# Kernel tuning notes

Measured on AMD Instinct MI355X. Metric: run time of the kernel, lower is better.

## Reference

```python
import jax, jax.numpy as jnp
import numpy as np

SLOPE = 25.0  # snntorch surrogate.fast_sigmoid default slope
NUM_STEPS = 15

@jax.custom_vjp
def spike(x):
    # Heaviside forward, fast-sigmoid surrogate backward
    return (x > 0).astype(x.dtype)

def _spike_fwd(x):
    return spike(x), x

def _spike_bwd(x, g):
    return (g / (SLOPE * jnp.abs(x) + 1.0) ** 2,)

spike.defvjp(_spike_fwd, _spike_bwd)


def setup_inputs() -> dict:
    p, hidden, B = 97, 512, 32768
    key = jax.random.key(0)
    ks = jax.random.split(key, 6)
    s1 = 1.0 / np.sqrt(2 * hidden)
    s2 = 1.0 / np.sqrt(hidden)
    return {
        "x": jax.random.randint(ks[0], (B, 2), 0, p, dtype=jnp.int64 if jax.config.jax_enable_x64 else jnp.int32),
        "embed_w": jax.random.normal(ks[1], (p, hidden), jnp.float32),
        "W1": jax.random.uniform(ks[2], (hidden, 2 * hidden), jnp.float32, -s1, s1),
        "b1": jax.random.uniform(ks[3], (hidden,), jnp.float32, -s1, s1),
        "W2": jax.random.uniform(ks[4], (p, hidden), jnp.float32, -s2, s2),
        "b2": jax.random.uniform(ks[5], (p,), jnp.float32, -s2, s2),
        "beta1": jnp.float32(0.85),
        "beta2": jnp.float32(0.85),
        "thr1": jnp.float32(1.0),
        "thr2": jnp.float32(1.0),
    }


def reference(x, embed_w, W1, b1, W2, b2, beta1, beta2, thr1, thr2):
    # parameter clamps (done in-place under no_grad in torch)
    beta1 = jnp.clip(beta1, 0.1, 0.9)
    beta2 = jnp.clip(beta2, 0.1, 0.9)
    thr1 = jnp.maximum(thr1, 0.1)
    thr2 = jnp.maximum(thr2, 0.1)

    B = x.shape[0]
    hidden = embed_w.shape[1]
    p = W2.shape[0]

    emb = embed_w[x].reshape(B, 2 * hidden)          # [B, 2H]
    cur1 = emb @ W1.T + b1                           # constant across steps [B, H]

    def step(carry, _):
        mem1, mem2 = carry
        # lif1: Leaky, reset_mechanism='subtract'; reset computed from prev mem (detached)
        reset = jax.lax.stop_gradient((mem1 - thr1 > 0).astype(mem1.dtype))
        mem1 = jnp.clip(beta1, 0.0, 1.0) * mem1 + cur1 - reset * thr1
        spk1 = spike(mem1 - thr1)                    # [B, H]
        cur2 = spk1 @ W2.T + b2                      # [B, p]
        # lif2: reset_mechanism='none'
        mem2 = jnp.clip(beta2, 0.0, 1.0) * mem2 + cur2
        return (mem1, mem2), None

    mem1 = jnp.zeros((B, hidden), cur1.dtype)
    mem2 = jnp.zeros((B, p), cur1.dtype)
    (mem1, mem2), _ = jax.lax.scan(step, (mem1, mem2), None, length=NUM_STEPS)
    return mem2  # final membrane potential of output layer
```

## Files before the change

kernel.cpp:

```cpp
#include <hip/hip_runtime.h>
#include <cstddef>

#define PMOD 97
#define HID 512
#define NPAIR 9409
#define NSTEPS 15

typedef __attribute__((ext_vector_type(8))) short short8;
typedef __attribute__((ext_vector_type(4))) short short4_t;
typedef __attribute__((ext_vector_type(4))) float f32x4;

static __device__ __forceinline__ unsigned short f2bf_rn(float f) {
    unsigned u = __float_as_uint(f);
    u += 0x7FFFu + ((u >> 16) & 1u);
    return (unsigned short)(u >> 16);
}
static __device__ __forceinline__ float bf2f(unsigned short h) {
    return __uint_as_float(((unsigned)h) << 16);
}

__global__ __launch_bounds__(256) void k_cvt(const float* __restrict__ W1,
                                             const float* __restrict__ embed,
                                             const float* __restrict__ W2,
                                             short* __restrict__ w1hi,
                                             short* __restrict__ w1lo,
                                             short* __restrict__ ehi,
                                             short* __restrict__ elo,
                                             short* __restrict__ w2bf) {
    const int idx = blockIdx.x * 256 + threadIdx.x;
    if (idx < 131072) {
        const float4 v = ((const float4*)W1)[idx];
        const float vv[4] = {v.x, v.y, v.z, v.w};
        short4_t h4, l4;
#pragma unroll
        for (int q = 0; q < 4; ++q) {
            const unsigned short hb = f2bf_rn(vv[q]);
            h4[q] = (short)hb;
            l4[q] = (short)f2bf_rn(vv[q] - bf2f(hb));
        }
        *(short4_t*)(w1hi + idx * 4) = h4;
        *(short4_t*)(w1lo + idx * 4) = l4;
    } else if (idx < 143488) {
        const int k = idx - 131072;
        const float4 v = ((const float4*)embed)[k];
        const float vv[4] = {v.x, v.y, v.z, v.w};
        short4_t h4, l4;
#pragma unroll
        for (int q = 0; q < 4; ++q) {
            const unsigned short hb = f2bf_rn(vv[q]);
            h4[q] = (short)hb;
            l4[q] = (short)f2bf_rn(vv[q] - bf2f(hb));
        }
        *(short4_t*)(ehi + k * 4) = h4;
        *(short4_t*)(elo + k * 4) = l4;
    } else if (idx < 155904) {
        const int k = idx - 143488;
        const float4 v = ((const float4*)W2)[k];
        const float vv[4] = {v.x, v.y, v.z, v.w};
        short4_t h4;
#pragma unroll
        for (int q = 0; q < 4; ++q) h4[q] = (short)f2bf_rn(vv[q]);
        *(short4_t*)(w2bf + k * 4) = h4;
    }
}

__global__ __launch_bounds__(256) void k_abm(const short* __restrict__ ehi,
                                             const short* __restrict__ elo,
                                             const short* __restrict__ w1hi,
                                             const short* __restrict__ w1lo,
                                             const float* __restrict__ b1,
                                             float* __restrict__ Ap,
                                             float* __restrict__ Bm) {
    __shared__ f32x4 red[3][4][64];

    const int t = threadIdx.x;
    const int lane = t & 63;
    const int kq = t >> 6;
    const int mt = blockIdx.x >> 4;
    const int ng = blockIdx.x & 15;

    int e = mt * 16 + (lane & 15);
    if (e > PMOD - 1) e = PMOD - 1;
    const int kbase = kq * 128 + (lane >> 4) * 8;

    f32x4 acc[4];
#pragma unroll
    for (int nt = 0; nt < 4; ++nt) acc[nt] = (f32x4){0.f, 0.f, 0.f, 0.f};

#pragma unroll
    for (int kt = 0; kt < 4; ++kt) {
        const int k = kbase + kt * 32;
        const short8 ahi = *(const short8*)(ehi + (size_t)e * HID + k);
        const short8 alo = *(const short8*)(elo + (size_t)e * HID + k);
#pragma unroll
        for (int nt = 0; nt < 4; ++nt) {
            const int n = ng * 64 + nt * 16 + (lane & 15);
            const int h = n & 511;
            const int half = n >> 9;
            const size_t boff = (size_t)h * 1024 + half * HID + k;
            const short8 bhi = *(const short8*)(w1hi + boff);
            const short8 blo = *(const short8*)(w1lo + boff);
            acc[nt] = __builtin_amdgcn_mfma_f32_16x16x32_bf16(ahi, bhi, acc[nt], 0, 0, 0);
            acc[nt] = __builtin_amdgcn_mfma_f32_16x16x32_bf16(alo, bhi, acc[nt], 0, 0, 0);
            acc[nt] = __builtin_amdgcn_mfma_f32_16x16x32_bf16(ahi, blo, acc[nt], 0, 0, 0);
        }
    }

    if (kq != 0) {
#pragma unroll
        for (int nt = 0; nt < 4; ++nt) red[kq - 1][nt][lane] = acc[nt];
    }
    __syncthreads();
    if (kq == 0) {
#pragma unroll
        for (int nt = 0; nt < 4; ++nt) {
            f32x4 a = acc[nt];
            a += red[0][nt][lane];
            a += red[1][nt][lane];
            a += red[2][nt][lane];
            const int n = ng * 64 + nt * 16 + (lane & 15);
            const int h = n & 511;
            const int half = n >> 9;
            const float bias = half ? 0.f : b1[h];
#pragma unroll
            for (int reg = 0; reg < 4; ++reg) {
                const int er = mt * 16 + (lane >> 4) * 4 + reg;
                if (er < PMOD) {
                    if (half == 0) Ap[(size_t)er * HID + h] = a[reg] + bias;
                    else           Bm[(size_t)er * HID + h] = a[reg];
                }
            }
        }
    }
}

__global__ __launch_bounds__(256) void k_pairs(const float* __restrict__ Ap,
                                               const float* __restrict__ Bm,
                                               const short* __restrict__ w2bf,
                                               const float* __restrict__ b2,
                                               const float* __restrict__ pbeta1,
                                               const float* __restrict__ pbeta2,
                                               const float* __restrict__ pthr1,
                                               float* __restrict__ pairOut) {
    __shared__ f32x4 red[3][7][64];

    const float beta1 = fminf(fmaxf(pbeta1[0], 0.1f), 0.9f);
    const float beta2 = fminf(fmaxf(pbeta2[0], 0.1f), 0.9f);
    const float thr   = fmaxf(pthr1[0], 0.1f);

    const int t = threadIdx.x;
    const int lane = t & 63;
    const int kq = t >> 6;
    const int pblk = blockIdx.x * 16;

    const int pid0 = pblk + (lane & 15);
    const int pid  = (pid0 < NPAIR) ? pid0 : (NPAIR - 1);
    const unsigned i = (unsigned)pid / PMOD;
    const unsigned j = (unsigned)pid - i * PMOD;
    const int kbase = kq * 128 + (lane >> 4) * 8;

    f32x4 acc[7];
#pragma unroll
    for (int nt = 0; nt < 7; ++nt) acc[nt] = (f32x4){0.f, 0.f, 0.f, 0.f};

#pragma unroll
    for (int kt = 0; kt < 4; ++kt) {
        const int k = kbase + kt * 32;
        const float* ap = Ap + (size_t)i * HID + k;
        const float* bp = Bm + (size_t)j * HID + k;
        const float4 a0 = *(const float4*)ap;
        const float4 a1 = *(const float4*)(ap + 4);
        const float4 g0 = *(const float4*)bp;
        const float4 g1 = *(const float4*)(bp + 4);
        float c[8] = {a0.x + g0.x, a0.y + g0.y, a0.z + g0.z, a0.w + g0.w,
                      a1.x + g1.x, a1.y + g1.y, a1.z + g1.z, a1.w + g1.w};
        float cm[8], m[8], w[8];
        bool sb[8];
#pragma unroll
        for (int q = 0; q < 8; ++q) {
            cm[q] = c[q] - thr; m[q] = 0.f; w[q] = 0.f; sb[q] = false;
        }
        for (int s = 0; s < NSTEPS; ++s) {
#pragma unroll
            for (int q = 0; q < 8; ++q) {
                const float cadj = sb[q] ? cm[q] : c[q];
                m[q] = fmaf(beta1, m[q], cadj);
                sb[q] = m[q] > thr;
                w[q] = fmaf(beta2, w[q], sb[q] ? 1.f : 0.f);
            }
        }
        short8 af;
#pragma unroll
        for (int q = 0; q < 8; ++q) af[q] = (short)f2bf_rn(w[q]);

#pragma unroll
        for (int nt = 0; nt < 7; ++nt) {
            const int o0 = nt * 16 + (lane & 15);
            const int oc = (o0 < PMOD) ? o0 : (PMOD - 1);
            const short8 bf = *(const short8*)(w2bf + (size_t)oc * HID + k);
            acc[nt] = __builtin_amdgcn_mfma_f32_16x16x32_bf16(af, bf, acc[nt], 0, 0, 0);
        }
    }

    if (kq != 0) {
#pragma unroll
        for (int nt = 0; nt < 7; ++nt) red[kq - 1][nt][lane] = acc[nt];
    }
    __syncthreads();
    if (kq == 0) {
        float S = 0.f;
#pragma unroll
        for (int s = 0; s < NSTEPS; ++s) S = fmaf(beta2, S, 1.f);
#pragma unroll
        for (int nt = 0; nt < 7; ++nt) {
            f32x4 a = acc[nt];
            a += red[0][nt][lane];
            a += red[1][nt][lane];
            a += red[2][nt][lane];
            const int o = nt * 16 + (lane & 15);
            if (o < PMOD) {
                const float bias = b2[o] * S;
#pragma unroll
                for (int reg = 0; reg < 4; ++reg) {
                    const int prow = pblk + (lane >> 4) * 4 + reg;
                    if (prow < NPAIR)
                        pairOut[(size_t)prow * PMOD + o] = a[reg] + bias;
                }
            }
        }
    }
}

__global__ __launch_bounds__(256) void k_scatter(const int* __restrict__ x,
                                                 const float* __restrict__ pairOut,
                                                 float* __restrict__ out,
                                                 int total) {
    const unsigned idx = blockIdx.x * 256u + threadIdx.x;
    if (idx >= (unsigned)total) return;
    const unsigned b = idx / PMOD;
    const unsigned o = idx - b * PMOD;
    const int pid = x[2 * b] * PMOD + x[2 * b + 1];
    out[idx] = pairOut[(size_t)pid * PMOD + o];
}

extern "C" void kernel_launch(void* const* d_in, const int* in_sizes, int n_in,
                              void* d_out, int out_size, void* d_ws, size_t ws_size,
                              hipStream_t stream) {
    const int*   x     = (const int*)d_in[0];
    const float* embed = (const float*)d_in[1];
    const float* W1    = (const float*)d_in[2];
    const float* b1    = (const float*)d_in[3];
    const float* W2    = (const float*)d_in[4];
    const float* b2    = (const float*)d_in[5];
    const float* beta1 = (const float*)d_in[6];
    const float* beta2 = (const float*)d_in[7];
    const float* thr1  = (const float*)d_in[8];

    float* out = (float*)d_out;
    const int B = in_sizes[0] / 2;

    char* ws = (char*)d_ws;
    short* w1hi    = (short*)(ws);
    short* w1lo    = (short*)(ws + 1048576);
    short* ehi     = (short*)(ws + 2097152);
    short* elo     = (short*)(ws + 2196480);
    float* pairOut = (float*)(ws);
    short* w2bf    = (short*)(ws + 3650816);
    float* Ap      = (float*)(ws + 3750144);
    float* Bm      = (float*)(ws + 3948800);

    k_cvt<<<609, 256, 0, stream>>>(W1, embed, W2, w1hi, w1lo, ehi, elo, w2bf);

    k_abm<<<112, 256, 0, stream>>>(ehi, elo, w1hi, w1lo, b1, Ap, Bm);

    const int nblk = (NPAIR + 15) / 16;
    k_pairs<<<nblk, 256, 0, stream>>>(Ap, Bm, w2bf, b2, beta1, beta2, thr1, pairOut);

    const int total = B * PMOD;
    k_scatter<<<(total + 255) / 256, 256, 0, stream>>>(x, pairOut, out, total);
}
```

Before: 48.87 us.

## Fuse weight conversion into A/B GEMM and split pair kernel across eight waves

Removes the separate conversion kernel. k_abm now splits embed and W1 into bf16 hi/lo on the fly and also converts W2, using four times more blocks with one N-tile each. k_pairs moves to 512 threads: each wave runs the LIF recurrence for two K-slices and stores the spike-rate fragments in shared memory. The waves then split the output MFMA work across K-quarters and output-tile halves. This saves one launch and the workspace round trip, and spreads the serial recurrence over more waves. The cost is redundant hi/lo conversion across blocks and an extra barrier.

Result: faster. 46.27 us (-5.3%).

```diff
diff --git a/kernel.cpp b/kernel.cpp
--- a/kernel.cpp
+++ b/kernel.cpp
@@ -18,123 +18,82 @@
 static __device__ __forceinline__ float bf2f(unsigned short h) {
     return __uint_as_float(((unsigned)h) << 16);
 }
-
-__global__ __launch_bounds__(256) void k_cvt(const float* __restrict__ W1,
-                                             const float* __restrict__ embed,
+static __device__ __forceinline__ void split_hilo(const float* __restrict__ p,
+                                                  short8& hi, short8& lo) {
+    const float4 v0 = *(const float4*)p;
+    const float4 v1 = *(const float4*)(p + 4);
+    const float vv[8] = {v0.x, v0.y, v0.z, v0.w, v1.x, v1.y, v1.z, v1.w};
+#pragma unroll
+    for (int q = 0; q < 8; ++q) {
+        const unsigned short hb = f2bf_rn(vv[q]);
+        hi[q] = (short)hb;
+        lo[q] = (short)f2bf_rn(vv[q] - bf2f(hb));
+    }
+}
+
+__global__ __launch_bounds__(256) void k_abm(const float* __restrict__ embed,
+                                             const float* __restrict__ W1,
                                              const float* __restrict__ W2,
-                                             short* __restrict__ w1hi,
-                                             short* __restrict__ w1lo,
-                                             short* __restrict__ ehi,
-                                             short* __restrict__ elo,
-                                             short* __restrict__ w2bf) {
-    const int idx = blockIdx.x * 256 + threadIdx.x;
-    if (idx < 131072) {
-        const float4 v = ((const float4*)W1)[idx];
-        const float vv[4] = {v.x, v.y, v.z, v.w};
-        short4_t h4, l4;
-#pragma unroll
-        for (int q = 0; q < 4; ++q) {
-            const unsigned short hb = f2bf_rn(vv[q]);
-            h4[q] = (short)hb;
-            l4[q] = (short)f2bf_rn(vv[q] - bf2f(hb));
-        }
-        *(short4_t*)(w1hi + idx * 4) = h4;
-        *(short4_t*)(w1lo + idx * 4) = l4;
-    } else if (idx < 143488) {
-        const int k = idx - 131072;
-        const float4 v = ((const float4*)embed)[k];
-        const float vv[4] = {v.x, v.y, v.z, v.w};
-        short4_t h4, l4;
-#pragma unroll
-        for (int q = 0; q < 4; ++q) {
-            const unsigned short hb = f2bf_rn(vv[q]);
-            h4[q] = (short)hb;
-            l4[q] = (short)f2bf_rn(vv[q] - bf2f(hb));
-        }
-        *(short4_t*)(ehi + k * 4) = h4;
-        *(short4_t*)(elo + k * 4) = l4;
-    } else if (idx < 155904) {
-        const int k = idx - 143488;
-        const float4 v = ((const float4*)W2)[k];
-        const float vv[4] = {v.x, v.y, v.z, v.w};
-        short4_t h4;
-#pragma unroll
-        for (int q = 0; q < 4; ++q) h4[q] = (short)f2bf_rn(vv[q]);
-        *(short4_t*)(w2bf + k * 4) = h4;
-    }
-}
-
-__global__ __launch_bounds__(256) void k_abm(const short* __restrict__ ehi,
-                                             const short* __restrict__ elo,
-                                             const short* __restrict__ w1hi,
-                                             const short* __restrict__ w1lo,
                                              const float* __restrict__ b1,
+                                             short* __restrict__ w2bf,
                                              float* __restrict__ Ap,
                                              float* __restrict__ Bm) {
-    __shared__ f32x4 red[3][4][64];
+    __shared__ f32x4 red[3][64];
 
     const int t = threadIdx.x;
     const int lane = t & 63;
     const int kq = t >> 6;
-    const int mt = blockIdx.x >> 4;
-    const int ng = blockIdx.x & 15;
-
+
+    const int gid = blockIdx.x * 256 + t;
+    if (gid < PMOD * HID / 4) {
+        const float4 v = ((const float4*)W2)[gid];
+        const float vv[4] = {v.x, v.y, v.z, v.w};
+        short4_t h4;
+#pragma unroll
+        for (int q = 0; q < 4; ++q) h4[q] = (short)f2bf_rn(vv[q]);
+        *(short4_t*)(w2bf + gid * 4) = h4;
+    }
+
+    const int mt = blockIdx.x >> 6;
+    const int ng = blockIdx.x & 63;
     int e = mt * 16 + (lane & 15);
     if (e > PMOD - 1) e = PMOD - 1;
+    const int n = ng * 16 + (lane & 15);
+    const int h = n & 511;
+    const int half = n >> 9;
     const int kbase = kq * 128 + (lane >> 4) * 8;
 
-    f32x4 acc[4];
-#pragma unroll
-    for (int nt = 0; nt < 4; ++nt) acc[nt] = (f32x4){0.f, 0.f, 0.f, 0.f};
-
+    f32x4 acc = (f32x4){0.f, 0.f, 0.f, 0.f};
 #pragma unroll
     for (int kt = 0; kt < 4; ++kt) {
         const int k = kbase + kt * 32;
-        const short8 ahi = *(const short8*)(ehi + (size_t)e * HID + k);
-        const short8 alo = *(const short8*)(elo + (size_t)e * HID + k);
-#pragma unroll
-        for (int nt = 0; nt < 4; ++nt) {
-            const int n = ng * 64 + nt * 16 + (lane & 15);
-            const int h = n & 511;
-            const int half = n >> 9;
-            const size_t boff = (size_t)h * 1024 + half * HID + k;
-            const short8 bhi = *(const short8*)(w1hi + boff);
-            const short8 blo = *(const short8*)(w1lo + boff);
-            acc[nt] = __builtin_amdgcn_mfma_f32_16x16x32_bf16(ahi, bhi, acc[nt], 0, 0, 0);
-            acc[nt] = __builtin_amdgcn_mfma_f32_16x16x32_bf16(alo, bhi, acc[nt], 0, 0, 0);
-            acc[nt] = __builtin_amdgcn_mfma_f32_16x16x32_bf16(ahi, blo, acc[nt], 0, 0, 0);
-        }
-    }
-
-    if (kq != 0) {
-#pragma unroll
-        for (int nt = 0; nt < 4; ++nt) red[kq - 1][nt][lane] = acc[nt];
-    }
+        short8 ahi, alo, bhi, blo;
+        split_hilo(embed + (size_t)e * HID + k, ahi, alo);
+        split_hilo(W1 + (size_t)h * 1024 + half * HID + k, bhi, blo);
+        acc = __builtin_amdgcn_mfma_f32_16x16x32_bf16(ahi, bhi, acc, 0, 0, 0);
+        acc = __builtin_amdgcn_mfma_f32_16x16x32_bf16(alo, bhi, acc, 0, 0, 0);
+        acc = __builtin_amdgcn_mfma_f32_16x16x32_bf16(ahi, blo, acc, 0, 0, 0);
+    }
+
+    if (kq != 0) red[kq - 1][lane] = acc;
     __syncthreads();
     if (kq == 0) {
-#pragma unroll
-        for (int nt = 0; nt < 4; ++nt) {
-            f32x4 a = acc[nt];
-            a += red[0][nt][lane];
-            a += red[1][nt][lane];
-            a += red[2][nt][lane];
-            const int n = ng * 64 + nt * 16 + (lane & 15);
-            const int h = n & 511;
-            const int half = n >> 9;
-            const float bias = half ? 0.f : b1[h];
-#pragma unroll
-            for (int reg = 0; reg < 4; ++reg) {
-                const int er = mt * 16 + (lane >> 4) * 4 + reg;
-                if (er < PMOD) {
-                    if (half == 0) Ap[(size_t)er * HID + h] = a[reg] + bias;
-                    else           Bm[(size_t)er * HID + h] = a[reg];
-                }
-            }
-        }
-    }
-}
-
-__global__ __launch_bounds__(256) void k_pairs(const float* __restrict__ Ap,
+        acc += red[0][lane];
+        acc += red[1][lane];
+        acc += red[2][lane];
+        const float bias = half ? 0.f : b1[h];
+#pragma unroll
+        for (int reg = 0; reg < 4; ++reg) {
+            const int er = mt * 16 + (lane >> 4) * 4 + reg;
+            if (er < PMOD) {
+                if (half == 0) Ap[(size_t)er * HID + h] = acc[reg] + bias;
+                else           Bm[(size_t)er * HID + h] = acc[reg];
+            }
+        }
+    }
+}
+
+__global__ __launch_bounds__(512) void k_pairs(const float* __restrict__ Ap,
                                                const float* __restrict__ Bm,
                                                const short* __restrict__ w2bf,
                                                const float* __restrict__ b2,
@@ -142,7 +101,8 @@
                                                const float* __restrict__ pbeta2,
                                                const float* __restrict__ pthr1,
                                                float* __restrict__ pairOut) {
-    __shared__ f32x4 red[3][7][64];
+    __shared__ short8 wfrag[16][64];
+    __shared__ f32x4 red[2][3][4][64];
 
     const float beta1 = fminf(fmaxf(pbeta1[0], 0.1f), 0.9f);
     const float beta2 = fminf(fmaxf(pbeta2[0], 0.1f), 0.9f);
@@ -150,35 +110,31 @@
 
     const int t = threadIdx.x;
     const int lane = t & 63;
-    const int kq = t >> 6;
+    const int w = t >> 6;
     const int pblk = blockIdx.x * 16;
 
     const int pid0 = pblk + (lane & 15);
     const int pid  = (pid0 < NPAIR) ? pid0 : (NPAIR - 1);
     const unsigned i = (unsigned)pid / PMOD;
     const unsigned j = (unsigned)pid - i * PMOD;
-    const int kbase = kq * 128 + (lane >> 4) * 8;
-
-    f32x4 acc[7];
-#pragma unroll
-    for (int nt = 0; nt < 7; ++nt) acc[nt] = (f32x4){0.f, 0.f, 0.f, 0.f};
-
-#pragma unroll
-    for (int kt = 0; kt < 4; ++kt) {
-        const int k = kbase + kt * 32;
-        const float* ap = Ap + (size_t)i * HID + k;
-        const float* bp = Bm + (size_t)j * HID + k;
+
+#pragma unroll
+    for (int kk = 0; kk < 2; ++kk) {
+        const int kt = 2 * w + kk;
+        const int h = kt * 32 + (lane >> 4) * 8;
+        const float* ap = Ap + (size_t)i * HID + h;
+        const float* bp = Bm + (size_t)j * HID + h;
         const float4 a0 = *(const float4*)ap;
         const float4 a1 = *(const float4*)(ap + 4);
         const float4 g0 = *(const float4*)bp;
         const float4 g1 = *(const float4*)(bp + 4);
         float c[8] = {a0.x + g0.x, a0.y + g0.y, a0.z + g0.z, a0.w + g0.w,
                       a1.x + g1.x, a1.y + g1.y, a1.z + g1.z, a1.w + g1.w};
-        float cm[8], m[8], w[8];
+        float cm[8], m[8], wv[8];
         bool sb[8];
 #pragma unroll
         for (int q = 0; q < 8; ++q) {
-            cm[q] = c[q] - thr; m[q] = 0.f; w[q] = 0.f; sb[q] = false;
+            cm[q] = c[q] - thr; m[q] = 0.f; wv[q] = 0.f; sb[q] = false;
         }
         for (int s = 0; s < NSTEPS; ++s) {
 #pragma unroll
@@ -186,25 +142,45 @@
                 const float cadj = sb[q] ? cm[q] : c[q];
                 m[q] = fmaf(beta1, m[q], cadj);
                 sb[q] = m[q] > thr;
-                w[q] = fmaf(beta2, w[q], sb[q] ? 1.f : 0.f);
+                wv[q] = fmaf(beta2, wv[q], sb[q] ? 1.f : 0.f);
             }
         }
         short8 af;
 #pragma unroll
-        for (int q = 0; q < 8; ++q) af[q] = (short)f2bf_rn(w[q]);
-
-#pragma unroll
-        for (int nt = 0; nt < 7; ++nt) {
-            const int o0 = nt * 16 + (lane & 15);
-            const int oc = (o0 < PMOD) ? o0 : (PMOD - 1);
-            const short8 bf = *(const short8*)(w2bf + (size_t)oc * HID + k);
-            acc[nt] = __builtin_amdgcn_mfma_f32_16x16x32_bf16(af, bf, acc[nt], 0, 0, 0);
+        for (int q = 0; q < 8; ++q) af[q] = (short)f2bf_rn(wv[q]);
+        wfrag[kt][lane] = af;
+    }
+    __syncthreads();
+
+    const int kq = w & 3;
+    const int nh = w >> 2;
+    const int ntb = nh * 4;
+
+    f32x4 acc[4];
+#pragma unroll
+    for (int q = 0; q < 4; ++q) acc[q] = (f32x4){0.f, 0.f, 0.f, 0.f};
+
+#pragma unroll
+    for (int kk = 0; kk < 4; ++kk) {
+        const int kt = kq * 4 + kk;
+        const short8 af = wfrag[kt][lane];
+        const int k = kt * 32 + (lane >> 4) * 8;
+#pragma unroll
+        for (int q = 0; q < 4; ++q) {
+            const int nt = ntb + q;
+            if (nt < 7) {
+                const int o0 = nt * 16 + (lane & 15);
+                const int oc = (o0 < PMOD) ? o0 : (PMOD - 1);
+                const short8 bf = *(const short8*)(w2bf + (size_t)oc * HID + k);
+                acc[q] = __builtin_amdgcn_mfma_f32_16x16x32_bf16(af, bf, acc[q], 0, 0, 0);
+            }
         }
     }
 
     if (kq != 0) {
 #pragma unroll
-        for (int nt = 0; nt < 7; ++nt) red[kq - 1][nt][lane] = acc[nt];
+        for (int q = 0; q < 4; ++q)
+            if (ntb + q < 7) red[nh][kq - 1][q][lane] = acc[q];
     }
     __syncthreads();
     if (kq == 0) {
@@ -212,19 +188,22 @@
 #pragma unroll
         for (int s = 0; s < NSTEPS; ++s) S = fmaf(beta2, S, 1.f);
 #pragma unroll
-        for (int nt = 0; nt < 7; ++nt) {
-            f32x4 a = acc[nt];
-            a += red[0][nt][lane];
-            a += red[1][nt][lane];
-            a += red[2][nt][lane];
-            const int o = nt * 16 + (lane & 15);
-            if (o < PMOD) {
-                const float bias = b2[o] * S;
-#pragma unroll
-                for (int reg = 0; reg < 4; ++reg) {
-                    const int prow = pblk + (lane >> 4) * 4 + reg;
-                    if (prow < NPAIR)
-                        pairOut[(size_t)prow * PMOD + o] = a[reg] + bias;
+        for (int q = 0; q < 4; ++q) {
+            const int nt = ntb + q;
+            if (nt < 7) {
+                f32x4 a = acc[q];
+                a += red[nh][0][q][lane];
+                a += red[nh][1][q][lane];
+                a += red[nh][2][q][lane];
+                const int o = nt * 16 + (lane & 15);
+                if (o < PMOD) {
+                    const float bias = b2[o] * S;
+#pragma unroll
+                    for (int reg = 0; reg < 4; ++reg) {
+                        const int prow = pblk + (lane >> 4) * 4 + reg;
+                        if (prow < NPAIR)
+                            pairOut[(size_t)prow * PMOD + o] = a[reg] + bias;
+                    }
                 }
             }
         }
@@ -260,21 +239,15 @@
     const int B = in_sizes[0] / 2;
 
     char* ws = (char*)d_ws;
-    short* w1hi    = (short*)(ws);
-    short* w1lo    = (short*)(ws + 1048576);
-    short* ehi     = (short*)(ws + 2097152);
-    short* elo     = (short*)(ws + 2196480);
     float* pairOut = (float*)(ws);
     short* w2bf    = (short*)(ws + 3650816);
     float* Ap      = (float*)(ws + 3750144);
     float* Bm      = (float*)(ws + 3948800);
 
-    k_cvt<<<609, 256, 0, stream>>>(W1, embed, W2, w1hi, w1lo, ehi, elo, w2bf);
-
-    k_abm<<<112, 256, 0, stream>>>(ehi, elo, w1hi, w1lo, b1, Ap, Bm);
+    k_abm<<<448, 256, 0, stream>>>(embed, W1, W2, b1, w2bf, Ap, Bm);
 
     const int nblk = (NPAIR + 15) / 16;
-    k_pairs<<<nblk, 256, 0, stream>>>(Ap, Bm, w2bf, b2, beta1, beta2, thr1, pairOut);
+    k_pairs<<<nblk, 512, 0, stream>>>(Ap, Bm, w2bf, b2, beta1, beta2, thr1, pairOut);
 
     const int total = B * PMOD;
     k_scatter<<<(total + 255) / 256, 256, 0, stream>>>(x, pairOut, out, total);
```
